# Kernel optimization log

Hardware: AMD Instinct MI355X
Metric: run time of the kernel (lower is better)

The kernel has to match this reference:

```python
import jax, jax.numpy as jnp
import numpy as np

NUM_COMPONENTS = 32
RESOLUTION = 512
NUM_POINTS = 2_000_000


def setup_inputs() -> dict:
    key = jax.random.key(0)
    kp, k0, k1, k2 = jax.random.split(key, 4)
    # positions are grid_sample-style normalized coords in [-1, 1]
    positions = jax.random.uniform(kp, (NUM_POINTS, 3), jnp.float32, -1.0, 1.0)
    vec_x = jax.random.normal(k0, (NUM_COMPONENTS, RESOLUTION), jnp.float32)
    vec_y = jax.random.normal(k1, (NUM_COMPONENTS, RESOLUTION), jnp.float32)
    vec_z = jax.random.normal(k2, (NUM_COMPONENTS, RESOLUTION), jnp.float32)
    return {"positions": positions, "vec_x": vec_x, "vec_y": vec_y, "vec_z": vec_z}


def _sample_1d(vec, x):
    """1D bilinear lookup mimicking grid_sample(align_corners=True, padding='zeros').
    vec: [C, R] per-axis CP vectors; x: [N] coords in [-1, 1]. Returns [C, N]."""
    R = vec.shape[1]
    ix = (x + 1.0) * 0.5 * (R - 1)          # map [-1,1] -> [0, R-1]
    i0 = jnp.floor(ix)
    w1 = ix - i0                              # right-neighbor weight
    i0i = i0.astype(jnp.int32)
    i1i = i0i + 1

    def gather(idx):
        valid = (idx >= 0) & (idx < R)        # zero-padding outside the grid
        g = jnp.take(vec, jnp.clip(idx, 0, R - 1), axis=1)  # [C, N]
        return jnp.where(valid[None, :], g, 0.0)

    return gather(i0i) * (1.0 - w1)[None, :] + gather(i1i) * w1[None, :]


def reference(positions, vec_x, vec_y, vec_z):
    # positions: [..., 3]; unbind per axis, 1D-sample each CP vector set, product-reduce.
    batch_shape = positions.shape[:-1]
    flat = positions.reshape(-1, 3)
    fx = _sample_1d(vec_x, flat[:, 0])  # [C, N]
    fy = _sample_1d(vec_y, flat[:, 1])  # [C, N]
    fz = _sample_1d(vec_z, flat[:, 2])  # [C, N]
    feats = fx * fy * fz                 # elementwise product over axes, [C, N]
    return feats.T.reshape(*batch_shape, vec_x.shape[0])  # [..., C]
```

## Files before the change

### kernel.cpp

```cpp
#include <hip/hip_runtime.h>

#define NC 32
#define NR 512

__global__ __launch_bounds__(256) void transpose_vecs(
    const float* __restrict__ vx, const float* __restrict__ vy,
    const float* __restrict__ vz, float* __restrict__ tx,
    float* __restrict__ ty, float* __restrict__ tz) {
  int u = blockIdx.x * 256 + threadIdx.x;
  if (u >= 3 * NC * NR) return;
  int table = u >> 14;
  int e = u & (NC * NR - 1);
  int c = e >> 9;
  int r = e & (NR - 1);
  const float* src = (table == 0) ? vx : (table == 1) ? vy : vz;
  float* dst = (table == 0) ? tx : (table == 1) ? ty : tz;
  dst[r * NC + c] = src[e];
}

__device__ __forceinline__ float4 sample4_t(const float* __restrict__ t,
                                            float x, int c4) {
  float ix = (x + 1.0f) * 0.5f * (float)(NR - 1);
  float f = floorf(ix);
  float w = ix - f;
  int i0 = (int)f;
  int i1 = i0 + 1;
  float m0 = (i0 >= 0 && i0 < NR) ? (1.0f - w) : 0.0f;
  float m1 = (i1 >= 0 && i1 < NR) ? w : 0.0f;
  int ci0 = min(max(i0, 0), NR - 1);
  int ci1 = min(max(i1, 0), NR - 1);
  float4 v0 = *(const float4*)(t + ci0 * NC + c4);
  float4 v1 = *(const float4*)(t + ci1 * NC + c4);
  float4 r;
  r.x = v0.x * m0 + v1.x * m1;
  r.y = v0.y * m0 + v1.y * m1;
  r.z = v0.z * m0 + v1.z * m1;
  r.w = v0.w * m0 + v1.w * m1;
  return r;
}

__device__ __forceinline__ float4 sample4_u(const float* __restrict__ t,
                                            float x, int c4) {
  float ix = (x + 1.0f) * 0.5f * (float)(NR - 1);
  float f = floorf(ix);
  float w = ix - f;
  int i0 = (int)f;
  int i1 = i0 + 1;
  float m0 = (i0 >= 0 && i0 < NR) ? (1.0f - w) : 0.0f;
  float m1 = (i1 >= 0 && i1 < NR) ? w : 0.0f;
  int ci0 = min(max(i0, 0), NR - 1);
  int ci1 = min(max(i1, 0), NR - 1);
  float4 r;
  float* rp = (float*)&r;
  for (int j = 0; j < 4; ++j) {
    float v0 = t[(c4 + j) * NR + ci0];
    float v1 = t[(c4 + j) * NR + ci1];
    rp[j] = v0 * m0 + v1 * m1;
  }
  return r;
}

template <bool TRANSPOSED>
__global__ __launch_bounds__(256) void cp_encode(
    const float* __restrict__ pos, const float* __restrict__ tx,
    const float* __restrict__ ty, const float* __restrict__ tz,
    float* __restrict__ out, int npts) {
  int t = blockIdx.x * 256 + threadIdx.x;
  int p = t >> 3;
  if (p >= npts) return;
  int c4 = (t & 7) * 4;

  float x = pos[3 * p + 0];
  float y = pos[3 * p + 1];
  float z = pos[3 * p + 2];

  float4 fx, fy, fz;
  if (TRANSPOSED) {
    fx = sample4_t(tx, x, c4);
    fy = sample4_t(ty, y, c4);
    fz = sample4_t(tz, z, c4);
  } else {
    fx = sample4_u(tx, x, c4);
    fy = sample4_u(ty, y, c4);
    fz = sample4_u(tz, z, c4);
  }

  float4 r;
  r.x = fx.x * fy.x * fz.x;
  r.y = fx.y * fy.y * fz.y;
  r.z = fx.z * fy.z * fz.z;
  r.w = fx.w * fy.w * fz.w;
  *(float4*)(out + (long long)p * NC + c4) = r;
}

extern "C" void kernel_launch(void* const* d_in, const int* in_sizes, int n_in,
                              void* d_out, int out_size, void* d_ws,
                              size_t ws_size, hipStream_t stream) {
  const float* pos = (const float*)d_in[0];
  const float* vx = (const float*)d_in[1];
  const float* vy = (const float*)d_in[2];
  const float* vz = (const float*)d_in[3];
  float* out = (float*)d_out;
  int npts = in_sizes[0] / 3;

  const size_t tbytes = (size_t)3 * NC * NR * sizeof(float);
  int total_threads = npts * 8;
  int blocks = (total_threads + 255) / 256;

  if (ws_size >= tbytes) {
    float* tx = (float*)d_ws;
    float* ty = tx + NC * NR;
    float* tz = ty + NC * NR;
    int tb = (3 * NC * NR + 255) / 256;
    transpose_vecs<<<tb, 256, 0, stream>>>(vx, vy, vz, tx, ty, tz);
    cp_encode<true><<<blocks, 256, 0, stream>>>(pos, tx, ty, tz, out, npts);
  } else {
    cp_encode<false><<<blocks, 256, 0, stream>>>(pos, vx, vy, vz, out, npts);
  }
}
```

Baseline: 316.4 us.

## Stage half-channel lookup tables in LDS with persistent chunked blocks

```diff
diff --git a/kernel.cpp b/kernel.cpp
--- a/kernel.cpp
+++ b/kernel.cpp
@@ -2,6 +2,12 @@
 
 #define NC 32
 #define NR 512
+#define HC 16
+#define NCHUNK 256
+#define BLK 1024
+
+#define LDS_FLOATS (3 * NR * HC + HC)
+#define LDS_BYTES (LDS_FLOATS * 4)
 
 __global__ __launch_bounds__(256) void transpose_vecs(
     const float* __restrict__ vx, const float* __restrict__ vy,
@@ -15,28 +21,78 @@
   int r = e & (NR - 1);
   const float* src = (table == 0) ? vx : (table == 1) ? vy : vz;
   float* dst = (table == 0) ? tx : (table == 1) ? ty : tz;
-  dst[r * NC + c] = src[e];
+  dst[((c >> 4) << 13) + (r << 4) + (c & (HC - 1))] = src[e];
 }
 
-__device__ __forceinline__ float4 sample4_t(const float* __restrict__ t,
-                                            float x, int c4) {
-  float ix = (x + 1.0f) * 0.5f * (float)(NR - 1);
+__device__ __forceinline__ float4 lerp4(const float* __restrict__ t,
+                                        float x, int j4) {
+  float ix = fmaf(x, 0.5f * (NR - 1), 0.5f * (NR - 1));
+  ix = fminf(fmaxf(ix, 0.0f), (float)(NR - 1));
   float f = floorf(ix);
   float w = ix - f;
   int i0 = (int)f;
-  int i1 = i0 + 1;
-  float m0 = (i0 >= 0 && i0 < NR) ? (1.0f - w) : 0.0f;
-  float m1 = (i1 >= 0 && i1 < NR) ? w : 0.0f;
-  int ci0 = min(max(i0, 0), NR - 1);
-  int ci1 = min(max(i1, 0), NR - 1);
-  float4 v0 = *(const float4*)(t + ci0 * NC + c4);
-  float4 v1 = *(const float4*)(t + ci1 * NC + c4);
+  const float* a = t + (i0 << 4) + j4;
+  float4 v0 = *(const float4*)a;
+  float4 v1 = *(const float4*)(a + HC);
   float4 r;
-  r.x = v0.x * m0 + v1.x * m1;
-  r.y = v0.y * m0 + v1.y * m1;
-  r.z = v0.z * m0 + v1.z * m1;
-  r.w = v0.w * m0 + v1.w * m1;
+  r.x = fmaf(w, v1.x - v0.x, v0.x);
+  r.y = fmaf(w, v1.y - v0.y, v0.y);
+  r.z = fmaf(w, v1.z - v0.z, v0.z);
+  r.w = fmaf(w, v1.w - v0.w, v0.w);
   return r;
+}
+
+__global__ __launch_bounds__(BLK) void cp_encode_lds(
+    const float* __restrict__ pos, const float* __restrict__ tx,
+    const float* __restrict__ ty, const float* __restrict__ tz,
+    float* __restrict__ out, int npts, int chunk_pts) {
+  extern __shared__ float lds[];
+  int tid = threadIdx.x;
+  int base_p = blockIdx.x * chunk_pts;
+  int pend = min(base_p + chunk_pts, npts);
+  int iters = (chunk_pts + (BLK / 4) - 1) >> 8;
+
+  int j4 = (tid & 3) << 2;
+  int pofs = tid >> 2;
+
+  for (int h = 0; h < 2; ++h) {
+    __syncthreads();
+    for (int u = tid; u < 3 * NR * 4; u += BLK) {
+      int a = u >> 11;
+      int rem = u & 2047;
+      const float* src = (a == 0) ? tx : (a == 1) ? ty : tz;
+      float4 v = *(const float4*)(src + (h << 13) + (rem << 2));
+      *(float4*)(&lds[(a << 13) + (rem << 2)]) = v;
+    }
+    if (h == 0 && tid < HC) lds[3 * NR * HC + tid] = 0.0f;
+    __syncthreads();
+
+    int p = base_p + pofs;
+    int pc = min(p, npts - 1);
+    float x = pos[3 * pc], y = pos[3 * pc + 1], z = pos[3 * pc + 2];
+
+    for (int it = 0; it < iters; ++it) {
+      int pn = p + (BLK / 4);
+      float xn = 0.f, yn = 0.f, zn = 0.f;
+      if (it + 1 < iters) {
+        int pcn = min(pn, npts - 1);
+        xn = pos[3 * pcn];
+        yn = pos[3 * pcn + 1];
+        zn = pos[3 * pcn + 2];
+      }
+      float4 fx = lerp4(lds, x, j4);
+      float4 fy = lerp4(lds + (NR * HC), y, j4);
+      float4 fz = lerp4(lds + 2 * (NR * HC), z, j4);
+      float4 r;
+      r.x = fx.x * fy.x * fz.x;
+      r.y = fx.y * fy.y * fz.y;
+      r.z = fx.z * fy.z * fz.z;
+      r.w = fx.w * fy.w * fz.w;
+      if (p < pend)
+        *(float4*)(out + (size_t)p * NC + h * HC + j4) = r;
+      p = pn; x = xn; y = yn; z = zn;
+    }
+  }
 }
 
 __device__ __forceinline__ float4 sample4_u(const float* __restrict__ t,
@@ -60,31 +116,20 @@
   return r;
 }
 
-template <bool TRANSPOSED>
-__global__ __launch_bounds__(256) void cp_encode(
-    const float* __restrict__ pos, const float* __restrict__ tx,
-    const float* __restrict__ ty, const float* __restrict__ tz,
+__global__ __launch_bounds__(256) void cp_encode_global(
+    const float* __restrict__ pos, const float* __restrict__ vx,
+    const float* __restrict__ vy, const float* __restrict__ vz,
     float* __restrict__ out, int npts) {
   int t = blockIdx.x * 256 + threadIdx.x;
   int p = t >> 3;
   if (p >= npts) return;
   int c4 = (t & 7) * 4;
-
   float x = pos[3 * p + 0];
   float y = pos[3 * p + 1];
   float z = pos[3 * p + 2];
-
-  float4 fx, fy, fz;
-  if (TRANSPOSED) {
-    fx = sample4_t(tx, x, c4);
-    fy = sample4_t(ty, y, c4);
-    fz = sample4_t(tz, z, c4);
-  } else {
-    fx = sample4_u(tx, x, c4);
-    fy = sample4_u(ty, y, c4);
-    fz = sample4_u(tz, z, c4);
-  }
-
+  float4 fx = sample4_u(vx, x, c4);
+  float4 fy = sample4_u(vy, y, c4);
+  float4 fz = sample4_u(vz, z, c4);
   float4 r;
   r.x = fx.x * fy.x * fz.x;
   r.y = fx.y * fy.y * fz.y;
@@ -104,17 +149,25 @@
   int npts = in_sizes[0] / 3;
 
   const size_t tbytes = (size_t)3 * NC * NR * sizeof(float);
-  int total_threads = npts * 8;
-  int blocks = (total_threads + 255) / 256;
 
   if (ws_size >= tbytes) {
+    static int lds_attr_set = 0;
+    if (!lds_attr_set) {
+      hipFuncSetAttribute((const void*)cp_encode_lds,
+                          hipFuncAttributeMaxDynamicSharedMemorySize,
+                          LDS_BYTES);
+      lds_attr_set = 1;
+    }
     float* tx = (float*)d_ws;
     float* ty = tx + NC * NR;
     float* tz = ty + NC * NR;
     int tb = (3 * NC * NR + 255) / 256;
     transpose_vecs<<<tb, 256, 0, stream>>>(vx, vy, vz, tx, ty, tz);
-    cp_encode<true><<<blocks, 256, 0, stream>>>(pos, tx, ty, tz, out, npts);
+    int chunk_pts = (npts + NCHUNK - 1) / NCHUNK;
+    cp_encode_lds<<<NCHUNK, BLK, LDS_BYTES, stream>>>(pos, tx, ty, tz, out,
+                                                      npts, chunk_pts);
   } else {
-    cp_encode<false><<<blocks, 256, 0, stream>>>(pos, vx, vy, vz, out, npts);
+    int blocks = (npts * 8 + 255) / 256;
+    cp_encode_global<<<blocks, 256, 0, stream>>>(pos, vx, vy, vz, out, npts);
   }
 }
```

Result: slower. 357.8 us (+13.1%).
